# Kernel tuning notes

Measured on AMD Instinct MI355X. Metric: run time of the kernel, lower is better.

## Reference

```python
import jax, jax.numpy as jnp
import numpy as np

# Module hyperparameters (match init_kwargs)
B = 131072          # batch
D_IN = 256          # input_dim
D_OUT = 256         # output_dim
K = 8               # num_nanocolumns
CHUNK = D_OUT // K  # per-nanocolumn output dim = 32
GAIN = 1.0          # alignment_gain buffer
THRESH = 0.3        # alignment_threshold buffer


def _l2norm(v, axis):
    # torch F.normalize(p=2): v / max(||v||, eps)
    return v / jnp.maximum(jnp.linalg.norm(v, axis=axis, keepdims=True), 1e-12)


def setup_inputs() -> dict:
    key = jax.random.key(0)
    ks = jax.random.split(key, 8)
    x = jax.random.normal(ks[0], (B, D_IN), jnp.float32)
    # input_projection: nn.Linear(D_IN, D_IN)
    Wp = jax.random.normal(ks[1], (D_IN, D_IN), jnp.float32) / np.sqrt(D_IN).astype(np.float32)
    bp = jnp.zeros((D_IN,), jnp.float32)
    # per-nanocolumn params, stacked over K
    pre = jax.random.normal(ks[2], (K, D_IN), jnp.float32)        # pre_synaptic_rim
    post = jax.random.normal(ks[3], (K, CHUNK), jnp.float32)      # post_synaptic_psd95
    Wc = jax.random.normal(ks[4], (K, CHUNK, D_IN), jnp.float32) * 0.01  # synaptic_weights
    # output_integration: nn.Linear(D_OUT, D_OUT)
    Wo = jax.random.normal(ks[5], (D_OUT, D_OUT), jnp.float32) / np.sqrt(D_OUT).astype(np.float32)
    bo = jnp.zeros((D_OUT,), jnp.float32)
    return {"x": x, "Wp": Wp, "bp": bp, "pre": pre, "post": post, "Wc": Wc, "Wo": Wo, "bo": bo}


def reference(x, Wp, bp, pre, post, Wc, Wo, bo):
    # forward with learning_enabled=False, allocation_mask = ones
    m = min(D_IN, CHUNK)  # compute_alignment truncates to min length
    proj = x @ Wp.T + bp                                   # [B, D_IN]
    # per-column alignment score: sigmoid(<norm(pre[:m]), norm(post[:m])> * gain)
    sim = jnp.sum(_l2norm(pre[:, :m], 1) * _l2norm(post[:, :m], 1), axis=1)  # [K]
    align = jax.nn.sigmoid(sim * GAIN)                      # [K]
    # dynamic threshold routing: inactive columns contribute zeros
    gate = jnp.where(align >= THRESH, align, 0.0)           # [K]
    # effective_weights = W * align; output = proj @ W.T, all K columns at once
    col = jnp.einsum('bi,koi->bko', proj, Wc) * gate[None, :, None]  # [B, K, CHUNK]
    combined = col.reshape(x.shape[0], D_OUT)               # concat over columns
    out = combined @ Wo.T + bo                              # output_integration
    alignments = align * (align >= THRESH).astype(x.dtype)
    allocation_mask = jnp.ones((K,), x.dtype)
    return (out, combined, alignments, allocation_mask)
```

## Files before the change

### kernel.cpp

```cpp
#include <hip/hip_runtime.h>
#include <hip/hip_bf16.h>
#include <cstdint>


#define BATCH 131072
#define TAIL ((size_t)2 * BATCH * 256)

typedef unsigned short u16;
typedef __attribute__((ext_vector_type(8))) short short8;
typedef __attribute__((ext_vector_type(4))) float floatx4;

__device__ __forceinline__ short f2bf(float f) {
    union { float f; unsigned u; } v; v.f = f;
    unsigned u = v.u;
    u += 0x7fffu + ((u >> 16) & 1u);
    return (short)(u >> 16);
}

__global__ void k_align(const float* __restrict__ pre, const float* __restrict__ post,
                        float* __restrict__ gate_ws, float* __restrict__ out_tail) {
    int k = threadIdx.x;
    if (k < 8) {
        float na = 0.f, nb = 0.f, dp = 0.f;
        for (int i = 0; i < 32; ++i) {
            float a = pre[k * 256 + i], b = post[k * 32 + i];
            na += a * a; nb += b * b; dp += a * b;
        }
        float denom = fmaxf(sqrtf(na), 1e-12f) * fmaxf(sqrtf(nb), 1e-12f);
        float sim = dp / denom;
        float align = 1.f / (1.f + expf(-sim));
        float gate = (align >= 0.3f) ? align : 0.f;
        gate_ws[k] = gate;
        out_tail[k] = gate;
        out_tail[8 + k] = 1.f;
    }
}

__global__ __launch_bounds__(256) void k_makeA(
        const float* __restrict__ Wc, const float* __restrict__ Wp,
        const float* __restrict__ bp, const float* __restrict__ gate_ws,
        float* __restrict__ A, float* __restrict__ bias512, u16* __restrict__ Wbig) {
    int j = blockIdx.x, t = threadIdx.x;
    __shared__ float wc[256];
    __shared__ float red[256];
    float g = gate_ws[j >> 5];
    float v = Wc[j * 256 + t];
    wc[t] = v;
    red[t] = v * bp[t];
    __syncthreads();
    for (int s = 128; s > 0; s >>= 1) {
        if (t < s) red[t] += red[t + s];
        __syncthreads();
    }
    if (t == 0) bias512[256 + j] = g * red[0];
    float acc = 0.f;
#pragma unroll 16
    for (int i = 0; i < 256; ++i) acc += wc[i] * Wp[i * 256 + t];
    acc *= g;
    A[j * 256 + t] = acc;
    Wbig[(256 + j) * 256 + t] = (u16)f2bf(acc);
}

__global__ __launch_bounds__(256) void k_makeB2(
        const float* __restrict__ Wo, const float* __restrict__ bo,
        const float* __restrict__ A, float* __restrict__ bias512,
        u16* __restrict__ Wbig) {
    int tt = blockIdx.x, t = threadIdx.x;
    __shared__ float wo[256];
    __shared__ float red[256];
    float v = Wo[tt * 256 + t];
    wo[t] = v;
    red[t] = v * bias512[256 + t];
    __syncthreads();
    for (int s = 128; s > 0; s >>= 1) {
        if (t < s) red[t] += red[t + s];
        __syncthreads();
    }
    if (t == 0) bias512[tt] = red[0] + bo[tt];
    float acc = 0.f;
#pragma unroll 16
    for (int i = 0; i < 256; ++i) acc += wo[i] * A[i * 256 + t];
    Wbig[tt * 256 + t] = (u16)f2bf(acc);
}

#define AS3(p) ((__attribute__((address_space(3))) void*)(p))
#define AS1(p) ((const __attribute__((address_space(1))) void*)(p))

__global__ __launch_bounds__(256, 2) void k_gemm(
        const float* __restrict__ x, const u16* __restrict__ Wbig,
        const float* __restrict__ bias512, float* __restrict__ out) {
    __shared__ float sA[128 * 32];
    __shared__ u16  sB[128 * 32];

    const int tid = threadIdx.x;
    const int wave = tid >> 6, lane = tid & 63;
    const int lr = lane & 15, quad = lane >> 4;
    const int b = blockIdx.x;
    const int mtile = ((b >> 5) << 3) + (b & 7);
    const int ntile = (b >> 3) & 3;
    const int m0 = mtile * 128, n0 = ntile * 128;
    const int wm = wave >> 1, wn = wave & 1;

    floatx4 acc[4][4];
#pragma unroll
    for (int i = 0; i < 4; ++i)
#pragma unroll
        for (int j = 0; j < 4; ++j) acc[i][j] = (floatx4)0.f;

    float biasj[4];
#pragma unroll
    for (int j = 0; j < 4; ++j) biasj[j] = bias512[n0 + wn * 64 + j * 16 + lr];

    const float* xg = x + (size_t)(m0 + (tid >> 3)) * 256 + (tid & 7) * 4;
    const u16*  wg = Wbig + (size_t)(n0 + (tid >> 2)) * 256 + (tid & 3) * 8;
    char* sAb = (char*)sA;
    char* sBb = (char*)sB;

    for (int kk = 0; kk < 8; ++kk) {
        const int k0 = kk * 32;
#pragma unroll
        for (int r = 0; r < 4; ++r)
            __builtin_amdgcn_global_load_lds(AS1(xg + k0 + r * 32 * 256),
                                             AS3(sAb + wave * 1024 + r * 4096), 16, 0, 0);
#pragma unroll
        for (int r = 0; r < 2; ++r)
            __builtin_amdgcn_global_load_lds(AS1(wg + k0 + r * 64 * 256),
                                             AS3(sBb + wave * 1024 + r * 4096), 16, 0, 0);
        __syncthreads();

        short8 af[4], bfr[4];
#pragma unroll
        for (int i = 0; i < 4; ++i) {
            const float* p = sA + (wm * 64 + i * 16 + lr) * 32 + quad * 8;
            float4 u0 = *(const float4*)p;
            float4 u1 = *(const float4*)(p + 4);
            af[i][0] = f2bf(u0.x); af[i][1] = f2bf(u0.y);
            af[i][2] = f2bf(u0.z); af[i][3] = f2bf(u0.w);
            af[i][4] = f2bf(u1.x); af[i][5] = f2bf(u1.y);
            af[i][6] = f2bf(u1.z); af[i][7] = f2bf(u1.w);
        }
#pragma unroll
        for (int j = 0; j < 4; ++j) {
            const u16* p = sB + (wn * 64 + j * 16 + lr) * 32 + quad * 8;
            bfr[j] = *(const short8*)p;
        }
#pragma unroll
        for (int i = 0; i < 4; ++i)
#pragma unroll
            for (int j = 0; j < 4; ++j)
                acc[i][j] = __builtin_amdgcn_mfma_f32_16x16x32_bf16(af[i], bfr[j], acc[i][j], 0, 0, 0);
        __syncthreads();
    }

    float* obase = out + ((ntile < 2) ? (size_t)0 : ((size_t)BATCH * 256));
    const int ncol0 = n0 - ((ntile < 2) ? 0 : 256);
#pragma unroll
    for (int i = 0; i < 4; ++i) {
#pragma unroll
        for (int j = 0; j < 4; ++j) {
            const int col = ncol0 + wn * 64 + j * 16 + lr;
#pragma unroll
            for (int r = 0; r < 4; ++r) {
                const size_t row = (size_t)(m0 + wm * 64 + i * 16 + quad * 4 + r);
                obase[row * 256 + col] = acc[i][j][r] + biasj[j];
            }
        }
    }
}

extern "C" void kernel_launch(void* const* d_in, const int* in_sizes, int n_in,
                              void* d_out, int out_size, void* d_ws, size_t ws_size,
                              hipStream_t stream) {
    const float* x    = (const float*)d_in[0];
    const float* Wp   = (const float*)d_in[1];
    const float* bp   = (const float*)d_in[2];
    const float* pre  = (const float*)d_in[3];
    const float* post = (const float*)d_in[4];
    const float* Wc   = (const float*)d_in[5];
    const float* Wo   = (const float*)d_in[6];
    const float* bo   = (const float*)d_in[7];
    float* out = (float*)d_out;

    char* ws = (char*)d_ws;
    float* gate_ws = (float*)(ws);
    float* bias512 = (float*)(ws + 64);
    float* A       = (float*)(ws + 4096);
    u16*  Wbig     = (u16*)(ws + 4096 + 262144);

    float* out_tail = out + TAIL;

    k_align<<<dim3(1), dim3(64), 0, stream>>>(pre, post, gate_ws, out_tail);
    k_makeA<<<dim3(256), dim3(256), 0, stream>>>(Wc, Wp, bp, gate_ws, A, bias512, Wbig);
    k_makeB2<<<dim3(256), dim3(256), 0, stream>>>(Wo, bo, A, bias512, Wbig);
    k_gemm<<<dim3(4096), dim3(256), 0, stream>>>(x, Wbig, bias512, out);
}
```

Measured before the change: 419.7 us.

## Load GEMM operands directly from global into registers, drop LDS staging

The main GEMM no longer stages x and the weights through shared memory with per-step barriers. Each wave now loads its MFMA fragments straight from global memory into registers, with the loop over K fully unrolled. The change also switches to packed bf16 conversion, uses nontemporal stores for the output, and recomputes the gate inside k_makeA so it no longer depends on a workspace value. The goal is to remove barrier and LDS round-trip overhead on a memory-bound GEMM. In exchange, operand reuse across waves now depends on L1/L2 caching, and the direct loads are less coalesced (each lane reads 32 bytes per row).

```diff
diff --git a/kernel.cpp b/kernel.cpp
--- a/kernel.cpp
+++ b/kernel.cpp
@@ -17,37 +17,53 @@
     return (short)(u >> 16);
 }
 
+__device__ __forceinline__ unsigned cvt2(float lo, float hi) {
+#if __has_builtin(__builtin_amdgcn_cvt_pk_bf16_f32)
+    auto p = __builtin_amdgcn_cvt_pk_bf16_f32(lo, hi);
+    union { decltype(p) p; unsigned u; } c; c.p = p; return c.u;
+#else
+    union { float f; unsigned u; } a, b; a.f = lo; b.f = hi;
+    return __builtin_amdgcn_perm(b.u, a.u, 0x07060302);
+#endif
+}
+
+__device__ __forceinline__ float gate_for(const float* pre, const float* post, int kc) {
+    float na = 0.f, nb = 0.f, dp = 0.f;
+    for (int i = 0; i < 32; ++i) {
+        float a = pre[kc * 256 + i], b = post[kc * 32 + i];
+        na += a * a; nb += b * b; dp += a * b;
+    }
+    float denom = fmaxf(sqrtf(na), 1e-12f) * fmaxf(sqrtf(nb), 1e-12f);
+    float sim = dp / denom;
+    float align = 1.f / (1.f + expf(-sim));
+    return (align >= 0.3f) ? align : 0.f;
+}
+
 __global__ void k_align(const float* __restrict__ pre, const float* __restrict__ post,
-                        float* __restrict__ gate_ws, float* __restrict__ out_tail) {
+                        float* __restrict__ out_tail) {
     int k = threadIdx.x;
     if (k < 8) {
-        float na = 0.f, nb = 0.f, dp = 0.f;
-        for (int i = 0; i < 32; ++i) {
-            float a = pre[k * 256 + i], b = post[k * 32 + i];
-            na += a * a; nb += b * b; dp += a * b;
-        }
-        float denom = fmaxf(sqrtf(na), 1e-12f) * fmaxf(sqrtf(nb), 1e-12f);
-        float sim = dp / denom;
-        float align = 1.f / (1.f + expf(-sim));
-        float gate = (align >= 0.3f) ? align : 0.f;
-        gate_ws[k] = gate;
-        out_tail[k] = gate;
+        float g = gate_for(pre, post, k);
+        out_tail[k] = g;
         out_tail[8 + k] = 1.f;
     }
 }
 
 __global__ __launch_bounds__(256) void k_makeA(
         const float* __restrict__ Wc, const float* __restrict__ Wp,
-        const float* __restrict__ bp, const float* __restrict__ gate_ws,
+        const float* __restrict__ bp, const float* __restrict__ pre,
+        const float* __restrict__ post,
         float* __restrict__ A, float* __restrict__ bias512, u16* __restrict__ Wbig) {
     int j = blockIdx.x, t = threadIdx.x;
     __shared__ float wc[256];
     __shared__ float red[256];
-    float g = gate_ws[j >> 5];
+    __shared__ float gsh;
+    if (t == 0) gsh = gate_for(pre, post, j >> 5);
     float v = Wc[j * 256 + t];
     wc[t] = v;
     red[t] = v * bp[t];
     __syncthreads();
+    float g = gsh;
     for (int s = 128; s > 0; s >>= 1) {
         if (t < s) red[t] += red[t + s];
         __syncthreads();
@@ -83,15 +99,11 @@
     Wbig[tt * 256 + t] = (u16)f2bf(acc);
 }
 
-#define AS3(p) ((__attribute__((address_space(3))) void*)(p))
-#define AS1(p) ((const __attribute__((address_space(1))) void*)(p))
+union FragAB { short8 s; unsigned u[4]; };
 
 __global__ __launch_bounds__(256, 2) void k_gemm(
         const float* __restrict__ x, const u16* __restrict__ Wbig,
         const float* __restrict__ bias512, float* __restrict__ out) {
-    __shared__ float sA[128 * 32];
-    __shared__ u16  sB[128 * 32];
-
     const int tid = threadIdx.x;
     const int wave = tid >> 6, lane = tid & 63;
     const int lr = lane & 15, quad = lane >> 4;
@@ -107,50 +119,44 @@
 #pragma unroll
         for (int j = 0; j < 4; ++j) acc[i][j] = (floatx4)0.f;
 
+    const float* abase[4];
+#pragma unroll
+    for (int i = 0; i < 4; ++i)
+        abase[i] = x + (size_t)(m0 + wm * 64 + i * 16 + lr) * 256 + quad * 8;
+    const u16* bbase[4];
+#pragma unroll
+    for (int j = 0; j < 4; ++j)
+        bbase[j] = Wbig + (size_t)(n0 + wn * 64 + j * 16 + lr) * 256 + quad * 8;
+
+#pragma unroll
+    for (int kk = 0; kk < 8; ++kk) {
+        FragAB fa[4], fb[4];
+        float4 a0[4], a1[4];
+#pragma unroll
+        for (int i = 0; i < 4; ++i) {
+            a0[i] = *(const float4*)(abase[i] + kk * 32);
+            a1[i] = *(const float4*)(abase[i] + kk * 32 + 4);
+        }
+#pragma unroll
+        for (int j = 0; j < 4; ++j)
+            fb[j].s = *(const short8*)(bbase[j] + kk * 32);
+#pragma unroll
+        for (int i = 0; i < 4; ++i) {
+            fa[i].u[0] = cvt2(a0[i].x, a0[i].y);
+            fa[i].u[1] = cvt2(a0[i].z, a0[i].w);
+            fa[i].u[2] = cvt2(a1[i].x, a1[i].y);
+            fa[i].u[3] = cvt2(a1[i].z, a1[i].w);
+        }
+#pragma unroll
+        for (int i = 0; i < 4; ++i)
+#pragma unroll
+            for (int j = 0; j < 4; ++j)
+                acc[i][j] = __builtin_amdgcn_mfma_f32_16x16x32_bf16(fa[i].s, fb[j].s, acc[i][j], 0, 0, 0);
+    }
+
     float biasj[4];
 #pragma unroll
     for (int j = 0; j < 4; ++j) biasj[j] = bias512[n0 + wn * 64 + j * 16 + lr];
-
-    const float* xg = x + (size_t)(m0 + (tid >> 3)) * 256 + (tid & 7) * 4;
-    const u16*  wg = Wbig + (size_t)(n0 + (tid >> 2)) * 256 + (tid & 3) * 8;
-    char* sAb = (char*)sA;
-    char* sBb = (char*)sB;
-
-    for (int kk = 0; kk < 8; ++kk) {
-        const int k0 = kk * 32;
-#pragma unroll
-        for (int r = 0; r < 4; ++r)
-            __builtin_amdgcn_global_load_lds(AS1(xg + k0 + r * 32 * 256),
-                                             AS3(sAb + wave * 1024 + r * 4096), 16, 0, 0);
-#pragma unroll
-        for (int r = 0; r < 2; ++r)
-            __builtin_amdgcn_global_load_lds(AS1(wg + k0 + r * 64 * 256),
-                                             AS3(sBb + wave * 1024 + r * 4096), 16, 0, 0);
-        __syncthreads();
-
-        short8 af[4], bfr[4];
-#pragma unroll
-        for (int i = 0; i < 4; ++i) {
-            const float* p = sA + (wm * 64 + i * 16 + lr) * 32 + quad * 8;
-            float4 u0 = *(const float4*)p;
-            float4 u1 = *(const float4*)(p + 4);
-            af[i][0] = f2bf(u0.x); af[i][1] = f2bf(u0.y);
-            af[i][2] = f2bf(u0.z); af[i][3] = f2bf(u0.w);
-            af[i][4] = f2bf(u1.x); af[i][5] = f2bf(u1.y);
-            af[i][6] = f2bf(u1.z); af[i][7] = f2bf(u1.w);
-        }
-#pragma unroll
-        for (int j = 0; j < 4; ++j) {
-            const u16* p = sB + (wn * 64 + j * 16 + lr) * 32 + quad * 8;
-            bfr[j] = *(const short8*)p;
-        }
-#pragma unroll
-        for (int i = 0; i < 4; ++i)
-#pragma unroll
-            for (int j = 0; j < 4; ++j)
-                acc[i][j] = __builtin_amdgcn_mfma_f32_16x16x32_bf16(af[i], bfr[j], acc[i][j], 0, 0, 0);
-        __syncthreads();
-    }
 
     float* obase = out + ((ntile < 2) ? (size_t)0 : ((size_t)BATCH * 256));
     const int ncol0 = n0 - ((ntile < 2) ? 0 : 256);
@@ -162,7 +168,7 @@
 #pragma unroll
             for (int r = 0; r < 4; ++r) {
                 const size_t row = (size_t)(m0 + wm * 64 + i * 16 + quad * 4 + r);
-                obase[row * 256 + col] = acc[i][j][r] + biasj[j];
+                __builtin_nontemporal_store(acc[i][j][r] + biasj[j], &obase[row * 256 + col]);
             }
         }
     }
@@ -182,15 +188,14 @@
     float* out = (float*)d_out;
 
     char* ws = (char*)d_ws;
-    float* gate_ws = (float*)(ws);
     float* bias512 = (float*)(ws + 64);
     float* A       = (float*)(ws + 4096);
     u16*  Wbig     = (u16*)(ws + 4096 + 262144);
 
     float* out_tail = out + TAIL;
 
-    k_align<<<dim3(1), dim3(64), 0, stream>>>(pre, post, gate_ws, out_tail);
-    k_makeA<<<dim3(256), dim3(256), 0, stream>>>(Wc, Wp, bp, gate_ws, A, bias512, Wbig);
+    k_align<<<dim3(1), dim3(64), 0, stream>>>(pre, post, out_tail);
+    k_makeA<<<dim3(256), dim3(256), 0, stream>>>(Wc, Wp, bp, pre, post, A, bias512, Wbig);
     k_makeB2<<<dim3(256), dim3(256), 0, stream>>>(Wo, bo, A, bias512, Wbig);
     k_gemm<<<dim3(4096), dim3(256), 0, stream>>>(x, Wbig, bias512, out);
 }
```

Measured after the change: 557.6 us. 32.9% more time.
